# Kernel optimization log

Hardware: AMD Instinct MI355X
Metric: run time of the kernel (lower is better)

The kernel has to match this reference:

```python
import jax, jax.numpy as jnp
import numpy as np

N, E = 50000, 800000
IN_DIM, HID, H, L = 256, 128, 4, 2
HD = HID // H
EPS = 1e-5


def _bn(x, g, b):
    # training-mode BatchNorm1d: biased variance over batch dim, eps=1e-5
    m = x.mean(0)
    v = jnp.var(x, axis=0)
    return g * (x - m) * jax.lax.rsqrt(v + EPS) + b


def _seg_softmax(scores, dst, n):
    # scores: [E, H]; softmax over edges sharing the same dst node
    m = jax.ops.segment_max(scores, dst, num_segments=n)  # [N, H]
    e = jnp.exp(scores - m[dst])
    s = jax.ops.segment_sum(e, dst, num_segments=n)
    return e / s[dst]


def _attn_layer(h, src, dst, wq, bq, wk, bk, wv, bv, wo, bo):
    n = h.shape[0]
    scale = 1.0 / np.sqrt(HD)
    Q = (h @ wq + bq).reshape(n, H, HD)
    K = (h @ wk + bk).reshape(n, H, HD)
    V = (h @ wv + bv).reshape(n, H, HD)
    # per-edge scores: Q of src dotted with K of dst
    scores = jnp.einsum('ehd,ehd->eh', Q[src], K[dst]) * scale  # [E, H]
    attn = _seg_softmax(scores, dst, n)                         # [E, H]
    # weighted scatter-sum of V gathered at dst (faithful to source)
    out = jax.ops.segment_sum(attn[:, :, None] * V[dst], dst, num_segments=n)
    out = out.reshape(n, HID) @ wo + bo
    return jax.nn.relu(out)


def setup_inputs() -> dict:
    key = jax.random.key(0)
    ks = jax.random.split(key, 20)
    s = 0.05  # weight scale to keep activations tame
    inp = {
        'x': jax.random.normal(ks[0], (N, IN_DIM), jnp.float32),
        'edge_index': jax.random.randint(ks[1], (2, E), 0, N),
        'W_enc1': jax.random.normal(ks[2], (IN_DIM, HID), jnp.float32) * s,
        'b_enc1': jax.random.normal(ks[3], (HID,), jnp.float32) * s,
        'g1': jnp.ones((HID,), jnp.float32),
        'beta1': jnp.zeros((HID,), jnp.float32),
        'W_enc2': jax.random.normal(ks[4], (HID, HID), jnp.float32) * s,
        'b_enc2': jax.random.normal(ks[5], (HID,), jnp.float32) * s,
        'g2': jnp.ones((HID,), jnp.float32),
        'beta2': jnp.zeros((HID,), jnp.float32),
        'Wq': jax.random.normal(ks[6], (L, HID, HID), jnp.float32) * s,
        'bq': jax.random.normal(ks[7], (L, HID), jnp.float32) * s,
        'Wk': jax.random.normal(ks[8], (L, HID, HID), jnp.float32) * s,
        'bk': jax.random.normal(ks[9], (L, HID), jnp.float32) * s,
        'Wv': jax.random.normal(ks[10], (L, HID, HID), jnp.float32) * s,
        'bv': jax.random.normal(ks[11], (L, HID), jnp.float32) * s,
        'Wo': jax.random.normal(ks[12], (L, HID, HID), jnp.float32) * s,
        'bo': jax.random.normal(ks[13], (L, HID), jnp.float32) * s,
    }
    return inp


def reference(x, edge_index, W_enc1, b_enc1, g1, beta1, W_enc2, b_enc2, g2, beta2,
              Wq, bq, Wk, bk, Wv, bv, Wo, bo):
    src, dst = edge_index[0], edge_index[1]
    # encoder: Linear -> BN -> ReLU -> (dropout=id) -> Linear -> BN -> ReLU
    h = jax.nn.relu(_bn(x @ W_enc1 + b_enc1, g1, beta1))
    h = jax.nn.relu(_bn(h @ W_enc2 + b_enc2, g2, beta2))
    for i in range(L):
        h = _attn_layer(h, src, dst, Wq[i], bq[i], Wk[i], bk[i],
                        Wv[i], bv[i], Wo[i], bo[i])
    return h
```

## Files before the change

### kernel.cpp

```cpp
#include <hip/hip_runtime.h>

#define NN 50000
#define NE 800000
#define NB 782
#define TOTF 114688

typedef unsigned short u16;
typedef unsigned int u32;
typedef __attribute__((ext_vector_type(8))) short s8v;
typedef __attribute__((ext_vector_type(4))) float f4v;

__device__ __forceinline__ void split2(float f, u16& h, u16& lo) {
    u32 u = __float_as_uint(f);
    h = (u16)(u >> 16);
    float r = f - __uint_as_float(u & 0xFFFF0000u);
    lo = (u16)(__float_as_uint(r) >> 16);
}

__global__ void mask_scatter_k(const int* __restrict__ dst, float* __restrict__ mask) {
    int i = blockIdx.x * blockDim.x + threadIdx.x;
    if (i < NE) mask[dst[i]] = 1.0f;
}

__global__ void prep_w_k(const float* __restrict__ W1, const float* __restrict__ W2,
                         const float* __restrict__ Wv, const float* __restrict__ Wo,
                         u16* __restrict__ fh, u16* __restrict__ fl) {
    int idx = blockIdx.x * 256 + threadIdx.x;
    if (idx >= TOTF) return;
    const float* W;
    int local;
    if (idx < 32768) { W = W1; local = idx; }
    else {
        int t = idx - 32768;
        int m = t >> 14;
        local = t & 16383;
        if (m == 0) W = W2;
        else if (m == 1) W = Wv;
        else if (m == 2) W = Wo;
        else if (m == 3) W = Wv + 16384;
        else W = Wo + 16384;
    }
    int j = local & 7, l = (local >> 3) & 63, nt = (local >> 9) & 7, kc = local >> 12;
    int k = kc * 32 + ((l >> 4) << 3) + j;
    int n = nt * 16 + (l & 15);
    u16 h, lo;
    split2(W[k * 128 + n], h, lo);
    fh[idx] = h;
    fl[idx] = lo;
}

__global__ __launch_bounds__(64)
void redstats_k(const float* __restrict__ pst, float* __restrict__ st) {
    int c = blockIdx.x;
    float s = 0.f;
    for (int b = threadIdx.x; b < NB; b += 64) s += pst[(size_t)b * 256 + c];
    s += __shfl_xor(s, 1);  s += __shfl_xor(s, 2);  s += __shfl_xor(s, 4);
    s += __shfl_xor(s, 8);  s += __shfl_xor(s, 16); s += __shfl_xor(s, 32);
    if (threadIdx.x == 0) st[c] = s;
}

template<int KC, int FOLD, int STATS>
__global__ __launch_bounds__(256)
void mgemm_k(const float* __restrict__ A,
             const u16* __restrict__ fh, const u16* __restrict__ fl,
             const float* __restrict__ bias,
             const float* __restrict__ fst,
             const float* __restrict__ fg, const float* __restrict__ fbe,
             float* __restrict__ pst,
             float* __restrict__ C) {
    constexpr int K = KC * 32;
    __shared__ u16 Ah[64][K + 8];
    __shared__ u16 Al[64][K + 8];
    __shared__ float scl[128], shf[128];
    __shared__ float wsum[4][128], wsq[4][128];
    const int tid = threadIdx.x;
    const int l = tid & 63, w = tid >> 6;
    const int q = l >> 4, cc = l & 15;
    const int row0 = blockIdx.x * 64;

    if (FOLD && tid < 128) {
        float mean = fst[tid] * (1.0f / NN);
        float var = fst[128 + tid] * (1.0f / NN) - mean * mean;
        float rstd = rsqrtf(var + 1e-5f);
        float ga = fg[tid] * rstd;
        scl[tid] = ga;
        shf[tid] = fbe[tid] - mean * ga;
    }
    if (FOLD) __syncthreads();

#pragma unroll
    for (int i = 0; i < K / 16; ++i) {
        int lin = i * 64 + l;
        int r16 = lin / (K / 4);
        int c4 = (lin % (K / 4)) * 4;
        int gr = row0 + 16 * w + r16; if (gr > NN - 1) gr = NN - 1;
        float4 f = *(const float4*)(A + (size_t)gr * K + c4);
        float v[4] = {f.x, f.y, f.z, f.w};
        if (FOLD) {
#pragma unroll
            for (int m = 0; m < 4; ++m) {
                float t = v[m] * scl[c4 + m] + shf[c4 + m];
                v[m] = t > 0.f ? t : 0.f;
            }
        }
        int rl = 16 * w + r16;
#pragma unroll
        for (int m = 0; m < 4; ++m) {
            u16 h, lo; split2(v[m], h, lo);
            Ah[rl][c4 + m] = h;
            Al[rl][c4 + m] = lo;
        }
    }

    f4v zf = {0.f, 0.f, 0.f, 0.f};
    f4v acc[8];
#pragma unroll
    for (int nt = 0; nt < 8; ++nt) acc[nt] = zf;

#pragma unroll
    for (int kc = 0; kc < KC; ++kc) {
        int ks = kc * 32 + q * 8;
        s8v ah = *(const s8v*)&Ah[16 * w + cc][ks];
        s8v al = *(const s8v*)&Al[16 * w + cc][ks];
#pragma unroll
        for (int nt = 0; nt < 8; ++nt) {
            const int fo = (((kc * 8 + nt) * 64) + l) * 8;
            s8v bh = *(const s8v*)(fh + fo);
            s8v bl = *(const s8v*)(fl + fo);
            acc[nt] = __builtin_amdgcn_mfma_f32_16x16x32_bf16(ah, bh, acc[nt], 0, 0, 0);
            acc[nt] = __builtin_amdgcn_mfma_f32_16x16x32_bf16(ah, bl, acc[nt], 0, 0, 0);
            acc[nt] = __builtin_amdgcn_mfma_f32_16x16x32_bf16(al, bh, acc[nt], 0, 0, 0);
        }
    }

    float ps[8], pq[8];
#pragma unroll
    for (int nt = 0; nt < 8; ++nt) { ps[nt] = 0.f; pq[nt] = 0.f; }
#pragma unroll
    for (int nt = 0; nt < 8; ++nt) {
        float bb = bias[nt * 16 + cc];
#pragma unroll
        for (int r = 0; r < 4; ++r) {
            int gr = row0 + 16 * w + q * 4 + r;
            float val = acc[nt][r] + bb;
            if (gr < NN) {
                C[(size_t)gr * 128 + nt * 16 + cc] = val;
                if (STATS) { ps[nt] += val; pq[nt] += val * val; }
            }
        }
    }
    if (STATS) {
#pragma unroll
        for (int nt = 0; nt < 8; ++nt) {
            ps[nt] += __shfl_xor(ps[nt], 16); ps[nt] += __shfl_xor(ps[nt], 32);
            pq[nt] += __shfl_xor(pq[nt], 16); pq[nt] += __shfl_xor(pq[nt], 32);
        }
        if (l < 16) {
#pragma unroll
            for (int nt = 0; nt < 8; ++nt) {
                wsum[w][nt * 16 + l] = ps[nt];
                wsq[w][nt * 16 + l] = pq[nt];
            }
        }
        __syncthreads();
        if (tid < 128) {
            pst[(size_t)blockIdx.x * 256 + tid] =
                wsum[0][tid] + wsum[1][tid] + wsum[2][tid] + wsum[3][tid];
        } else {
            int c = tid - 128;
            pst[(size_t)blockIdx.x * 256 + tid] =
                wsq[0][c] + wsq[1][c] + wsq[2][c] + wsq[3][c];
        }
    }
}

__global__ __launch_bounds__(256)
void mmega_k(const float* __restrict__ X,
             const u16* __restrict__ fh, const u16* __restrict__ fl,
             const float* __restrict__ bv, const float* __restrict__ bo,
             const float* __restrict__ fst,
             const float* __restrict__ fg, const float* __restrict__ fbe,
             const float* __restrict__ mask, float* __restrict__ out) {
    __shared__ u16 Ah[64][136];
    __shared__ u16 Al[64][136];
    __shared__ float scl[128], shf[128];
    const int tid = threadIdx.x;
    const int l = tid & 63, w = tid >> 6;
    const int q = l >> 4, cc = l & 15;
    const int row0 = blockIdx.x * 64;

    if (tid < 128) {
        float mean = fst[tid] * (1.0f / NN);
        float var = fst[128 + tid] * (1.0f / NN) - mean * mean;
        float rstd = rsqrtf(var + 1e-5f);
        float ga = fg[tid] * rstd;
        scl[tid] = ga;
        shf[tid] = fbe[tid] - mean * ga;
    }
    __syncthreads();

    float rm[4];
#pragma unroll
    for (int r = 0; r < 4; ++r) {
        int gr = row0 + 16 * w + q * 4 + r;
        rm[r] = (gr < NN) ? mask[gr] : 0.f;
    }

#pragma unroll
    for (int i = 0; i < 8; ++i) {
        int lin = i * 64 + l;
        int r16 = lin >> 5;
        int c4 = (lin & 31) * 4;
        int gr = row0 + 16 * w + r16; if (gr > NN - 1) gr = NN - 1;
        float4 f = *(const float4*)(X + (size_t)gr * 128 + c4);
        float v[4] = {f.x, f.y, f.z, f.w};
        int rl = 16 * w + r16;
#pragma unroll
        for (int m = 0; m < 4; ++m) {
            float t = v[m] * scl[c4 + m] + shf[c4 + m];
            t = t > 0.f ? t : 0.f;
            u16 h, lo; split2(t, h, lo);
            Ah[rl][c4 + m] = h;
            Al[rl][c4 + m] = lo;
        }
    }

    f4v zf = {0.f, 0.f, 0.f, 0.f};
    for (int s = 0; s < 4; ++s) {
        const u16* WH = fh + s * 16384;
        const u16* WL = fl + s * 16384;
        const float* bp = (s == 0) ? bv : (s == 1) ? bo : (s == 2) ? (bv + 128) : (bo + 128);

        f4v acc[8];
#pragma unroll
        for (int nt = 0; nt < 8; ++nt) acc[nt] = zf;
#pragma unroll
        for (int kc = 0; kc < 4; ++kc) {
            int ks = kc * 32 + q * 8;
            s8v ah = *(const s8v*)&Ah[16 * w + cc][ks];
            s8v al = *(const s8v*)&Al[16 * w + cc][ks];
#pragma unroll
            for (int nt = 0; nt < 8; ++nt) {
                const int fo = (((kc * 8 + nt) * 64) + l) * 8;
                s8v bh = *(const s8v*)(WH + fo);
                s8v bl = *(const s8v*)(WL + fo);
                acc[nt] = __builtin_amdgcn_mfma_f32_16x16x32_bf16(ah, bh, acc[nt], 0, 0, 0);
                acc[nt] = __builtin_amdgcn_mfma_f32_16x16x32_bf16(ah, bl, acc[nt], 0, 0, 0);
                acc[nt] = __builtin_amdgcn_mfma_f32_16x16x32_bf16(al, bh, acc[nt], 0, 0, 0);
            }
        }

        if (s == 3) {
#pragma unroll
            for (int nt = 0; nt < 8; ++nt) {
                float bb = bp[nt * 16 + cc];
#pragma unroll
                for (int r = 0; r < 4; ++r) {
                    int gr = row0 + 16 * w + q * 4 + r;
                    if (gr < NN)
                        out[(size_t)gr * 128 + nt * 16 + cc] = fmaxf(acc[nt][r] + bb, 0.f);
                }
            }
        } else {
#pragma unroll
            for (int nt = 0; nt < 8; ++nt) {
                float bb = bp[nt * 16 + cc];
#pragma unroll
                for (int r = 0; r < 4; ++r) {
                    int rl = 16 * w + q * 4 + r;
                    float val = acc[nt][r] + bb;
                    val = (s == 1) ? fmaxf(val, 0.f) : val * rm[r];
                    u16 h, lo; split2(val, h, lo);
                    Ah[rl][nt * 16 + cc] = h;
                    Al[rl][nt * 16 + cc] = lo;
                }
            }
        }
    }
}

extern "C" void kernel_launch(void* const* d_in, const int* in_sizes, int n_in,
                              void* d_out, int out_size, void* d_ws, size_t ws_size,
                              hipStream_t stream) {
    const float* x   = (const float*)d_in[0];
    const int*   ei  = (const int*)d_in[1];
    const float* W1  = (const float*)d_in[2];
    const float* b1  = (const float*)d_in[3];
    const float* g1  = (const float*)d_in[4];
    const float* be1 = (const float*)d_in[5];
    const float* W2  = (const float*)d_in[6];
    const float* b2  = (const float*)d_in[7];
    const float* g2  = (const float*)d_in[8];
    const float* be2 = (const float*)d_in[9];
    const float* Wv  = (const float*)d_in[14];
    const float* bv  = (const float*)d_in[15];
    const float* Wo  = (const float*)d_in[16];
    const float* bo  = (const float*)d_in[17];

    float* out = (float*)d_out;

    char* ws = (char*)d_ws;
    float* buf  = (float*)(ws);
    float* mask = (float*)(ws + 25600000);
    float* st1  = (float*)(ws + 25800704);
    float* st2  = st1 + 256;
    u16*   fH   = (u16*)(ws + 25804800);
    u16*   fL   = fH + TOTF;
    float* pst  = (float*)(ws + 26263552);

    hipMemsetAsync(mask, 0, NN * sizeof(float), stream);
    mask_scatter_k<<<dim3((NE + 255) / 256), dim3(256), 0, stream>>>(ei + NE, mask);
    prep_w_k<<<dim3((TOTF + 255) / 256), dim3(256), 0, stream>>>(W1, W2, Wv, Wo, fH, fL);

    dim3 gg(NB), bb(256);
    mgemm_k<8, 0, 1><<<gg, bb, 0, stream>>>(x, fH, fL, b1,
                                            nullptr, nullptr, nullptr, pst, buf);
    redstats_k<<<dim3(256), dim3(64), 0, stream>>>(pst, st1);
    mgemm_k<4, 1, 1><<<gg, bb, 0, stream>>>(buf, fH + 32768, fL + 32768, b2,
                                            st1, g1, be1, pst, out);
    redstats_k<<<dim3(256), dim3(64), 0, stream>>>(pst, st2);
    mmega_k<<<gg, bb, 0, stream>>>(out, fH + 49152, fL + 49152, bv, bo,
                                   st2, g2, be2, mask, out);
}
```

Baseline: 245.0 us.

## Split GEMM tiles across 8 waves and chunk K to shrink LDS

Doubles the block to 512 threads so each 16-row slice is handled by two waves, each computing half the output columns with 4 accumulators instead of 8. The first encoder GEMM now stages its 256-wide K in two 128-wide LDS chunks, which caps shared memory at the 128-column footprint, and the stats scratch reuses the A tile. The aim is more waves in flight and less LDS per block to hide global and weight-load latency. The cost is extra block-wide barriers in the chunk loop and between stages of the fused attention kernel.

```diff
diff --git a/kernel.cpp b/kernel.cpp
--- a/kernel.cpp
+++ b/kernel.cpp
@@ -60,7 +60,7 @@
 }
 
 template<int KC, int FOLD, int STATS>
-__global__ __launch_bounds__(256)
+__global__ __launch_bounds__(512, 6)
 void mgemm_k(const float* __restrict__ A,
              const u16* __restrict__ fh, const u16* __restrict__ fl,
              const float* __restrict__ bias,
@@ -68,14 +68,14 @@
              const float* __restrict__ fg, const float* __restrict__ fbe,
              float* __restrict__ pst,
              float* __restrict__ C) {
-    constexpr int K = KC * 32;
-    __shared__ u16 Ah[64][K + 8];
-    __shared__ u16 Al[64][K + 8];
+    constexpr int KP = KC / 4;
+    __shared__ __align__(16) u16 Ah[64][136];
+    __shared__ __align__(16) u16 Al[64][136];
     __shared__ float scl[128], shf[128];
-    __shared__ float wsum[4][128], wsq[4][128];
     const int tid = threadIdx.x;
     const int l = tid & 63, w = tid >> 6;
     const int q = l >> 4, cc = l & 15;
+    const int sl = w >> 1, hf = w & 1;
     const int row0 = blockIdx.x * 64;
 
     if (FOLD && tid < 128) {
@@ -86,107 +86,111 @@
         scl[tid] = ga;
         shf[tid] = fbe[tid] - mean * ga;
     }
-    if (FOLD) __syncthreads();
-
-#pragma unroll
-    for (int i = 0; i < K / 16; ++i) {
-        int lin = i * 64 + l;
-        int r16 = lin / (K / 4);
-        int c4 = (lin % (K / 4)) * 4;
-        int gr = row0 + 16 * w + r16; if (gr > NN - 1) gr = NN - 1;
-        float4 f = *(const float4*)(A + (size_t)gr * K + c4);
-        float v[4] = {f.x, f.y, f.z, f.w};
-        if (FOLD) {
-#pragma unroll
-            for (int m = 0; m < 4; ++m) {
-                float t = v[m] * scl[c4 + m] + shf[c4 + m];
-                v[m] = t > 0.f ? t : 0.f;
-            }
-        }
-        int rl = 16 * w + r16;
-#pragma unroll
-        for (int m = 0; m < 4; ++m) {
-            u16 h, lo; split2(v[m], h, lo);
-            Ah[rl][c4 + m] = h;
-            Al[rl][c4 + m] = lo;
-        }
-    }
 
     f4v zf = {0.f, 0.f, 0.f, 0.f};
-    f4v acc[8];
-#pragma unroll
-    for (int nt = 0; nt < 8; ++nt) acc[nt] = zf;
-
-#pragma unroll
-    for (int kc = 0; kc < KC; ++kc) {
-        int ks = kc * 32 + q * 8;
-        s8v ah = *(const s8v*)&Ah[16 * w + cc][ks];
-        s8v al = *(const s8v*)&Al[16 * w + cc][ks];
-#pragma unroll
-        for (int nt = 0; nt < 8; ++nt) {
-            const int fo = (((kc * 8 + nt) * 64) + l) * 8;
-            s8v bh = *(const s8v*)(fh + fo);
-            s8v bl = *(const s8v*)(fl + fo);
-            acc[nt] = __builtin_amdgcn_mfma_f32_16x16x32_bf16(ah, bh, acc[nt], 0, 0, 0);
-            acc[nt] = __builtin_amdgcn_mfma_f32_16x16x32_bf16(ah, bl, acc[nt], 0, 0, 0);
-            acc[nt] = __builtin_amdgcn_mfma_f32_16x16x32_bf16(al, bh, acc[nt], 0, 0, 0);
-        }
-    }
-
-    float ps[8], pq[8];
-#pragma unroll
-    for (int nt = 0; nt < 8; ++nt) { ps[nt] = 0.f; pq[nt] = 0.f; }
-#pragma unroll
-    for (int nt = 0; nt < 8; ++nt) {
-        float bb = bias[nt * 16 + cc];
+    f4v acc[4];
+#pragma unroll
+    for (int t = 0; t < 4; ++t) acc[t] = zf;
+
+    for (int p = 0; p < KP; ++p) {
+        if (p > 0 || FOLD) __syncthreads();
+#pragma unroll
+        for (int it = 0; it < 4; ++it) {
+            int lin = tid + 512 * it;
+            int r = lin >> 5;
+            int c4 = (lin & 31) * 4;
+            int gr = row0 + r; if (gr > NN - 1) gr = NN - 1;
+            float4 f = *(const float4*)(A + (size_t)gr * (KC * 32) + p * 128 + c4);
+            float v[4] = {f.x, f.y, f.z, f.w};
+            if (FOLD) {
+#pragma unroll
+                for (int m = 0; m < 4; ++m) {
+                    float t = v[m] * scl[c4 + m] + shf[c4 + m];
+                    v[m] = t > 0.f ? t : 0.f;
+                }
+            }
+            ushort4 uh, ul;
+            split2(v[0], uh.x, ul.x); split2(v[1], uh.y, ul.y);
+            split2(v[2], uh.z, ul.z); split2(v[3], uh.w, ul.w);
+            *(ushort4*)&Ah[r][c4] = uh;
+            *(ushort4*)&Al[r][c4] = ul;
+        }
+        __syncthreads();
+#pragma unroll
+        for (int kc = 0; kc < 4; ++kc) {
+            int kcg = p * 4 + kc;
+            s8v ah = *(const s8v*)&Ah[16 * sl + cc][kc * 32 + q * 8];
+            s8v al = *(const s8v*)&Al[16 * sl + cc][kc * 32 + q * 8];
+#pragma unroll
+            for (int t = 0; t < 4; ++t) {
+                const int fo = kcg * 4096 + (4 * hf + t) * 512 + l * 8;
+                s8v bh = *(const s8v*)(fh + fo);
+                s8v bl = *(const s8v*)(fl + fo);
+                acc[t] = __builtin_amdgcn_mfma_f32_16x16x32_bf16(ah, bh, acc[t], 0, 0, 0);
+                acc[t] = __builtin_amdgcn_mfma_f32_16x16x32_bf16(ah, bl, acc[t], 0, 0, 0);
+                acc[t] = __builtin_amdgcn_mfma_f32_16x16x32_bf16(al, bh, acc[t], 0, 0, 0);
+            }
+        }
+    }
+
+    float ps[4], pq[4];
+#pragma unroll
+    for (int t = 0; t < 4; ++t) { ps[t] = 0.f; pq[t] = 0.f; }
+#pragma unroll
+    for (int t = 0; t < 4; ++t) {
+        int col = (4 * hf + t) * 16 + cc;
+        float bb = bias[col];
 #pragma unroll
         for (int r = 0; r < 4; ++r) {
-            int gr = row0 + 16 * w + q * 4 + r;
-            float val = acc[nt][r] + bb;
+            int gr = row0 + 16 * sl + q * 4 + r;
+            float val = acc[t][r] + bb;
             if (gr < NN) {
-                C[(size_t)gr * 128 + nt * 16 + cc] = val;
-                if (STATS) { ps[nt] += val; pq[nt] += val * val; }
+                C[(size_t)gr * 128 + col] = val;
+                if (STATS) { ps[t] += val; pq[t] += val * val; }
             }
         }
     }
     if (STATS) {
-#pragma unroll
-        for (int nt = 0; nt < 8; ++nt) {
-            ps[nt] += __shfl_xor(ps[nt], 16); ps[nt] += __shfl_xor(ps[nt], 32);
-            pq[nt] += __shfl_xor(pq[nt], 16); pq[nt] += __shfl_xor(pq[nt], 32);
+        __syncthreads();
+        float* wredS = (float*)&Ah[0][0];
+        float* wredQ = wredS + 512;
+#pragma unroll
+        for (int t = 0; t < 4; ++t) {
+            ps[t] += __shfl_xor(ps[t], 16); ps[t] += __shfl_xor(ps[t], 32);
+            pq[t] += __shfl_xor(pq[t], 16); pq[t] += __shfl_xor(pq[t], 32);
         }
         if (l < 16) {
 #pragma unroll
-            for (int nt = 0; nt < 8; ++nt) {
-                wsum[w][nt * 16 + l] = ps[nt];
-                wsq[w][nt * 16 + l] = pq[nt];
+            for (int t = 0; t < 4; ++t) {
+                int col = (4 * hf + t) * 16 + l;
+                wredS[sl * 128 + col] = ps[t];
+                wredQ[sl * 128 + col] = pq[t];
             }
         }
         __syncthreads();
-        if (tid < 128) {
+        if (tid < 256) {
+            int c = tid & 127;
+            const float* src = (tid < 128) ? wredS : wredQ;
             pst[(size_t)blockIdx.x * 256 + tid] =
-                wsum[0][tid] + wsum[1][tid] + wsum[2][tid] + wsum[3][tid];
-        } else {
-            int c = tid - 128;
-            pst[(size_t)blockIdx.x * 256 + tid] =
-                wsq[0][c] + wsq[1][c] + wsq[2][c] + wsq[3][c];
-        }
-    }
-}
-
-__global__ __launch_bounds__(256)
+                src[c] + src[128 + c] + src[256 + c] + src[384 + c];
+        }
+    }
+}
+
+__global__ __launch_bounds__(512, 6)
 void mmega_k(const float* __restrict__ X,
              const u16* __restrict__ fh, const u16* __restrict__ fl,
              const float* __restrict__ bv, const float* __restrict__ bo,
              const float* __restrict__ fst,
              const float* __restrict__ fg, const float* __restrict__ fbe,
              const float* __restrict__ mask, float* __restrict__ out) {
-    __shared__ u16 Ah[64][136];
-    __shared__ u16 Al[64][136];
+    __shared__ __align__(16) u16 Ah[64][136];
+    __shared__ __align__(16) u16 Al[64][136];
     __shared__ float scl[128], shf[128];
     const int tid = threadIdx.x;
     const int l = tid & 63, w = tid >> 6;
     const int q = l >> 4, cc = l & 15;
+    const int sl = w >> 1, hf = w & 1;
     const int row0 = blockIdx.x * 64;
 
     if (tid < 128) {
@@ -202,28 +206,30 @@
     float rm[4];
 #pragma unroll
     for (int r = 0; r < 4; ++r) {
-        int gr = row0 + 16 * w + q * 4 + r;
+        int gr = row0 + 16 * sl + q * 4 + r;
         rm[r] = (gr < NN) ? mask[gr] : 0.f;
     }
 
 #pragma unroll
-    for (int i = 0; i < 8; ++i) {
-        int lin = i * 64 + l;
-        int r16 = lin >> 5;
+    for (int it = 0; it < 4; ++it) {
+        int lin = tid + 512 * it;
+        int r = lin >> 5;
         int c4 = (lin & 31) * 4;
-        int gr = row0 + 16 * w + r16; if (gr > NN - 1) gr = NN - 1;
+        int gr = row0 + r; if (gr > NN - 1) gr = NN - 1;
         float4 f = *(const float4*)(X + (size_t)gr * 128 + c4);
         float v[4] = {f.x, f.y, f.z, f.w};
-        int rl = 16 * w + r16;
+        ushort4 uh, ul;
 #pragma unroll
         for (int m = 0; m < 4; ++m) {
             float t = v[m] * scl[c4 + m] + shf[c4 + m];
-            t = t > 0.f ? t : 0.f;
-            u16 h, lo; split2(t, h, lo);
-            Ah[rl][c4 + m] = h;
-            Al[rl][c4 + m] = lo;
-        }
-    }
+            v[m] = t > 0.f ? t : 0.f;
+        }
+        split2(v[0], uh.x, ul.x); split2(v[1], uh.y, ul.y);
+        split2(v[2], uh.z, ul.z); split2(v[3], uh.w, ul.w);
+        *(ushort4*)&Ah[r][c4] = uh;
+        *(ushort4*)&Al[r][c4] = ul;
+    }
+    __syncthreads();
 
     f4v zf = {0.f, 0.f, 0.f, 0.f};
     for (int s = 0; s < 4; ++s) {
@@ -231,50 +237,53 @@
         const u16* WL = fl + s * 16384;
         const float* bp = (s == 0) ? bv : (s == 1) ? bo : (s == 2) ? (bv + 128) : (bo + 128);
 
-        f4v acc[8];
-#pragma unroll
-        for (int nt = 0; nt < 8; ++nt) acc[nt] = zf;
+        f4v acc[4];
+#pragma unroll
+        for (int t = 0; t < 4; ++t) acc[t] = zf;
 #pragma unroll
         for (int kc = 0; kc < 4; ++kc) {
-            int ks = kc * 32 + q * 8;
-            s8v ah = *(const s8v*)&Ah[16 * w + cc][ks];
-            s8v al = *(const s8v*)&Al[16 * w + cc][ks];
-#pragma unroll
-            for (int nt = 0; nt < 8; ++nt) {
-                const int fo = (((kc * 8 + nt) * 64) + l) * 8;
+            s8v ah = *(const s8v*)&Ah[16 * sl + cc][kc * 32 + q * 8];
+            s8v al = *(const s8v*)&Al[16 * sl + cc][kc * 32 + q * 8];
+#pragma unroll
+            for (int t = 0; t < 4; ++t) {
+                const int fo = kc * 4096 + (4 * hf + t) * 512 + l * 8;
                 s8v bh = *(const s8v*)(WH + fo);
                 s8v bl = *(const s8v*)(WL + fo);
-                acc[nt] = __builtin_amdgcn_mfma_f32_16x16x32_bf16(ah, bh, acc[nt], 0, 0, 0);
-                acc[nt] = __builtin_amdgcn_mfma_f32_16x16x32_bf16(ah, bl, acc[nt], 0, 0, 0);
-                acc[nt] = __builtin_amdgcn_mfma_f32_16x16x32_bf16(al, bh, acc[nt], 0, 0, 0);
+                acc[t] = __builtin_amdgcn_mfma_f32_16x16x32_bf16(ah, bh, acc[t], 0, 0, 0);
+                acc[t] = __builtin_amdgcn_mfma_f32_16x16x32_bf16(ah, bl, acc[t], 0, 0, 0);
+                acc[t] = __builtin_amdgcn_mfma_f32_16x16x32_bf16(al, bh, acc[t], 0, 0, 0);
             }
         }
 
         if (s == 3) {
 #pragma unroll
-            for (int nt = 0; nt < 8; ++nt) {
-                float bb = bp[nt * 16 + cc];
+            for (int t = 0; t < 4; ++t) {
+                int col = (4 * hf + t) * 16 + cc;
+                float bb = bp[col];
 #pragma unroll
                 for (int r = 0; r < 4; ++r) {
-                    int gr = row0 + 16 * w + q * 4 + r;
+                    int gr = row0 + 16 * sl + q * 4 + r;
                     if (gr < NN)
-                        out[(size_t)gr * 128 + nt * 16 + cc] = fmaxf(acc[nt][r] + bb, 0.f);
+                        out[(size_t)gr * 128 + col] = fmaxf(acc[t][r] + bb, 0.f);
                 }
             }
         } else {
-#pragma unroll
-            for (int nt = 0; nt < 8; ++nt) {
-                float bb = bp[nt * 16 + cc];
+            __syncthreads();
+#pragma unroll
+            for (int t = 0; t < 4; ++t) {
+                int col = (4 * hf + t) * 16 + cc;
+                float bb = bp[col];
 #pragma unroll
                 for (int r = 0; r < 4; ++r) {
-                    int rl = 16 * w + q * 4 + r;
-                    float val = acc[nt][r] + bb;
+                    int rl = 16 * sl + q * 4 + r;
+                    float val = acc[t][r] + bb;
                     val = (s == 1) ? fmaxf(val, 0.f) : val * rm[r];
                     u16 h, lo; split2(val, h, lo);
-                    Ah[rl][nt * 16 + cc] = h;
-                    Al[rl][nt * 16 + cc] = lo;
+                    Ah[rl][col] = h;
+                    Al[rl][col] = lo;
                 }
             }
+            __syncthreads();
         }
     }
 }
@@ -312,7 +321,7 @@
     mask_scatter_k<<<dim3((NE + 255) / 256), dim3(256), 0, stream>>>(ei + NE, mask);
     prep_w_k<<<dim3((TOTF + 255) / 256), dim3(256), 0, stream>>>(W1, W2, Wv, Wo, fH, fL);
 
-    dim3 gg(NB), bb(256);
+    dim3 gg(NB), bb(512);
     mgemm_k<8, 0, 1><<<gg, bb, 0, stream>>>(x, fH, fL, b1,
                                             nullptr, nullptr, nullptr, pst, buf);
     redstats_k<<<dim3(256), dim3(64), 0, stream>>>(pst, st1);
```

New measurement: 227.3 us. 7.2% less time.
